# Optimization experiments

Measured on AMD Instinct MI355X. Metric: run time of the kernel, lower is better.

Reference implementation:

```python
import jax, jax.numpy as jnp
import numpy as np

N = 100000      # nodes
E = 3200000     # edges
F_IN = 78       # num_features_mol
F_GAT = 256     # mol_out_feats
HEADS = 2
F_HYP = 128     # mol_out_feats_hyper


def setup_inputs() -> dict:
    key = jax.random.key(0)
    ks = jax.random.split(key, 32)
    g = lambda k, s: jax.random.normal(k, s, dtype=jnp.float32) * 0.05
    inp = {}
    inp["mol_x"] = jax.random.normal(ks[0], (N, F_IN), dtype=jnp.float32)
    inp["mol_edge_index"] = jax.random.randint(ks[1], (2, E), 0, N)
    inp["hyper_edge"] = jax.random.randint(ks[2], (2, E), 0, N)
    # GAT layer 1 (78 -> 256, 2 heads, concat=False)
    inp["W1"] = g(ks[3], (F_IN, HEADS * F_GAT)); inp["as1"] = g(ks[4], (HEADS, F_GAT)); inp["ad1"] = g(ks[5], (HEADS, F_GAT)); inp["b1"] = jnp.zeros((F_GAT,), jnp.float32)
    # GAT layers 2,3 (256 -> 256)
    inp["W2"] = g(ks[6], (F_GAT, HEADS * F_GAT)); inp["as2"] = g(ks[7], (HEADS, F_GAT)); inp["ad2"] = g(ks[8], (HEADS, F_GAT)); inp["b2"] = jnp.zeros((F_GAT,), jnp.float32)
    inp["W3"] = g(ks[9], (F_GAT, HEADS * F_GAT)); inp["as3"] = g(ks[10], (HEADS, F_GAT)); inp["ad3"] = g(ks[11], (HEADS, F_GAT)); inp["b3"] = jnp.zeros((F_GAT,), jnp.float32)
    # GRU-style gating fusion
    inp["fc1_w"] = g(ks[12], (F_GAT, F_GAT)); inp["fc1_b"] = jnp.zeros((F_GAT,), jnp.float32)
    inp["fc2_w"] = g(ks[13], (F_GAT, F_GAT)); inp["fc2_b"] = jnp.zeros((F_GAT,), jnp.float32)
    inp["mol_bias"] = jax.random.uniform(ks[14], (1, F_GAT), jnp.float32, -0.2, 0.2)
    # HypergraphConv layers (334 -> 128 -> 128)
    inp["theta1"] = g(ks[15], (F_GAT + F_IN, F_HYP)); inp["hb1"] = jnp.zeros((F_HYP,), jnp.float32)
    inp["theta2"] = g(ks[16], (F_HYP, F_HYP)); inp["hb2"] = jnp.zeros((F_HYP,), jnp.float32)
    return inp


def _gat(x, src, dst, W, a_s, a_d, b):
    # PyG GATConv, heads=2, concat=False, eval mode (no dropout), self-loops pre-added in src/dst
    xh = (x @ W).reshape(N, HEADS, F_GAT)            # [N,H,C]
    a_src = (xh * a_s).sum(-1)                        # [N,H]
    a_dst = (xh * a_d).sum(-1)                        # [N,H]
    e = jax.nn.leaky_relu(a_src[src] + a_dst[dst], 0.2)  # [E',H]
    m = jax.ops.segment_max(e, dst, num_segments=N)
    ex = jnp.exp(e - m[dst])
    s = jax.ops.segment_sum(ex, dst, num_segments=N)
    alpha = ex / s[dst]                               # softmax over incoming edges
    out = jax.ops.segment_sum(xh[src] * alpha[:, :, None], dst, num_segments=N)
    return out.mean(axis=1) + b                       # concat=False -> head mean


def _hyper(x, node, edge, theta, b):
    # PyG HypergraphConv, use_attention=False: D^-1 H B^-1 H^T X Theta + b
    xt = x @ theta
    ones = jnp.ones((node.shape[0],), xt.dtype)
    D = jax.ops.segment_sum(ones, node, num_segments=N)
    B = jax.ops.segment_sum(ones, edge, num_segments=N)
    Dinv = jnp.where(D > 0, 1.0 / D, 0.0)
    Binv = jnp.where(B > 0, 1.0 / B, 0.0)
    ef = Binv[:, None] * jax.ops.segment_sum(xt[node], edge, num_segments=N)
    nf = Dinv[:, None] * jax.ops.segment_sum(ef[edge], node, num_segments=N)
    return nf + b


def _forward(mol_x, mol_edge_index, hyper_edge,
             W1, as1, ad1, b1, W2, as2, ad2, b2, W3, as3, ad3, b3,
             fc1_w, fc1_b, fc2_w, fc2_b, mol_bias, theta1, hb1, theta2, hb2):
    loops = jnp.arange(N, dtype=mol_edge_index.dtype)
    src = jnp.concatenate([mol_edge_index[0], loops])
    dst = jnp.concatenate([mol_edge_index[1], loops])
    hyper_x0 = jax.lax.stop_gradient(mol_x)  # .clone().detach()
    # layer 0
    h = jax.nn.relu(_gat(mol_x, src, dst, W1, as1, ad1, b1))
    # layer 1 (relu) + gate
    x = jax.nn.relu(_gat(h, src, dst, W2, as2, ad2, b2))
    z = jax.nn.sigmoid(x @ fc1_w.T + fc1_b + h @ fc2_w.T + fc2_b + mol_bias)
    h = z * x + (1.0 - z) * h
    # layer 2 (no relu) + gate
    x = _gat(h, src, dst, W3, as3, ad3, b3)
    z = jax.nn.sigmoid(x @ fc1_w.T + fc1_b + h @ fc2_w.T + fc2_b + mol_bias)
    h = z * x + (1.0 - z) * h
    # hypergraph branch (source uses mol_edge_index here, hyper_edge is unused)
    hx = jnp.concatenate([jax.lax.stop_gradient(h), hyper_x0], axis=1)
    node, edge = mol_edge_index[0], mol_edge_index[1]
    hx = jax.nn.relu(_hyper(hx, node, edge, theta1, hb1))
    hx = jax.nn.relu(_hyper(hx, node, edge, theta2, hb2))
    return jnp.concatenate([h, hx], axis=1)  # [N, 384]


def reference(mol_x, mol_edge_index, hyper_edge,
              W1, as1, ad1, b1, W2, as2, ad2, b2, W3, as3, ad3, b3,
              fc1_w, fc1_b, fc2_w, fc2_b, mol_bias, theta1, hb1, theta2, hb2):
    return _forward(mol_x, mol_edge_index, hyper_edge,
                    W1, as1, ad1, b1, W2, as2, ad2, b2, W3, as3, ad3, b3,
                    fc1_w, fc1_b, fc2_w, fc2_b, mol_bias, theta1, hb1, theta2, hb2)
```

## Files before the change

### kernel.cpp

```cpp
#include <hip/hip_runtime.h>

typedef unsigned short u16;
typedef __attribute__((ext_vector_type(8))) short short8v;
typedef __attribute__((ext_vector_type(8))) unsigned short ushort8v;
typedef __attribute__((ext_vector_type(4))) unsigned short ushort4v;
typedef __attribute__((ext_vector_type(4))) float f32x4;

__device__ __forceinline__ float bf2f(u16 u) {
    union { unsigned int i; float f; } v; v.i = ((unsigned int)u) << 16; return v.f;
}
__device__ __forceinline__ u16 f2bf(float f) {
    union { float f; unsigned int i; } v; v.f = f;
    unsigned int i = v.i;
    return (u16)((i + 0x7FFFu + ((i >> 16) & 1u)) >> 16);
}
__device__ __forceinline__ float leaky02(float x) { return x > 0.f ? x : 0.2f * x; }
__device__ __forceinline__ float load_in(const void* p, long i, int isbf) {
    return isbf ? bf2f(((const u16*)p)[i]) : ((const float*)p)[i];
}

__global__ void detect_kernel(const unsigned* __restrict__ w, int* __restrict__ flag) {
    __shared__ int cnt;
    int t = threadIdx.x;
    if (t == 0) cnt = 0;
    __syncthreads();
    unsigned x = w[t * 16];
    unsigned lo = x & 0xFFFFu;
    int e = (int)((x >> 7) & 0xFFu);
    int good = (lo == 0u) || (e >= 100 && e <= 140);
    atomicAdd(&cnt, good);
    __syncthreads();
    if (t == 0) *flag = (cnt > 128) ? 1 : 0;
}

#define CSR_NBK 1024

__global__ __launch_bounds__(256)
void bucket_count_kernel(const int* __restrict__ ei, int* __restrict__ bcs,
                         int* __restrict__ bcd, int E_, int n, int SH) {
    __shared__ int hs[CSR_NBK], hd[CSR_NBK];
    const int t = threadIdx.x;
    for (int i = t; i < CSR_NBK; i += 256) { hs[i] = 0; hd[i] = 0; }
    __syncthreads();
    const int e0 = blockIdx.x * 4096;
    #pragma unroll
    for (int k = 0; k < 16; ++k) {
        int e = e0 + k * 256 + t;
        if (e < E_) {
            int s = ei[e], d = ei[E_ + e];
            if ((unsigned)s >= (unsigned)n) s = 0;
            if ((unsigned)d >= (unsigned)n) d = 0;
            atomicAdd(&hs[s >> SH], 1);
            atomicAdd(&hd[d >> SH], 1);
        }
    }
    __syncthreads();
    for (int i = t; i < CSR_NBK; i += 256) {
        if (hs[i]) atomicAdd(&bcs[i], hs[i]);
        if (hd[i]) atomicAdd(&bcd[i], hd[i]);
    }
}

__global__ void scan_excl_kernel(const int* __restrict__ deg, int* __restrict__ ptr, int n) {
    __shared__ int s_woff[17];
    __shared__ int s_carry;
    const int t = threadIdx.x;
    const int lane = t & 63, wid = t >> 6;
    if (t == 0) s_carry = 0;
    __syncthreads();
    for (int base = 0; base < n; base += 1024) {
        int i = base + t;
        int v = (i < n) ? deg[i] : 0;
        int incl = v;
        #pragma unroll
        for (int d = 1; d < 64; d <<= 1) {
            int x = __shfl_up(incl, d, 64);
            if (lane >= d) incl += x;
        }
        if (lane == 63) s_woff[wid] = incl;
        __syncthreads();
        if (t == 0) {
            int run = 0;
            #pragma unroll
            for (int w = 0; w < 16; ++w) { int x = s_woff[w]; s_woff[w] = run; run += x; }
            s_woff[16] = run;
        }
        __syncthreads();
        int excl = s_carry + s_woff[wid] + incl - v;
        if (i < n) ptr[i] = excl;
        __syncthreads();
        if (t == 0) s_carry += s_woff[16];
        __syncthreads();
    }
    if (t == 0) ptr[n] = s_carry;
}

__global__ void copy2_kernel(const int* __restrict__ a, int* __restrict__ b,
                             const int* __restrict__ c, int* __restrict__ d2, int n) {
    int i = blockIdx.x * 256 + threadIdx.x;
    if (i < n) { b[i] = a[i]; d2[i] = c[i]; }
}

__global__ __launch_bounds__(256)
void partition_kernel(const int* __restrict__ ei, int* __restrict__ bcur_s,
                      int* __restrict__ bcur_d, int2* __restrict__ ps,
                      int2* __restrict__ pd, int E_, int n, int SH) {
    __shared__ int cs[CSR_NBK], cd[CSR_NBK], bs[CSR_NBK], bd[CSR_NBK];
    const int t = threadIdx.x;
    for (int i = t; i < CSR_NBK; i += 256) { cs[i] = 0; cd[i] = 0; }
    __syncthreads();
    const int e0 = blockIdx.x * 4096;
    int sv[16], dv[16];
    #pragma unroll
    for (int k = 0; k < 16; ++k) {
        int e = e0 + k * 256 + t;
        int s = -1, d = 0;
        if (e < E_) {
            s = ei[e]; d = ei[E_ + e];
            if ((unsigned)s >= (unsigned)n) s = 0;
            if ((unsigned)d >= (unsigned)n) d = 0;
            atomicAdd(&cs[s >> SH], 1);
            atomicAdd(&cd[d >> SH], 1);
        }
        sv[k] = (e < E_) ? s : -1;
        dv[k] = d;
    }
    __syncthreads();
    for (int i = t; i < CSR_NBK; i += 256) {
        bs[i] = cs[i] ? atomicAdd(&bcur_s[i], cs[i]) : 0;
        bd[i] = cd[i] ? atomicAdd(&bcur_d[i], cd[i]) : 0;
        cs[i] = 0; cd[i] = 0;
    }
    __syncthreads();
    #pragma unroll
    for (int k = 0; k < 16; ++k) {
        int s = sv[k];
        if (s < 0) continue;
        int d = dv[k];
        int p = bs[s >> SH] + atomicAdd(&cs[s >> SH], 1);
        ps[p] = make_int2(d, s);
        int q = bd[d >> SH] + atomicAdd(&cd[d >> SH], 1);
        pd[q] = make_int2(s, d);
    }
}

__global__ __launch_bounds__(256)
void fill_bucket_kernel(const int2* __restrict__ pairs, const int* __restrict__ bptr,
                        int* __restrict__ ptr, int* __restrict__ idx, int n, int SH) {
    __shared__ int cnt[256];
    __shared__ int wsum[5];
    const int b = blockIdx.x;
    const int n0 = b << SH;
    if (n0 >= n) return;
    const int nn = min(1 << SH, n - n0);
    const int t = threadIdx.x;
    cnt[t] = 0;
    __syncthreads();
    const int pbeg = bptr[b], pend = bptr[b + 1];
    for (int j = pbeg + t; j < pend; j += 256)
        atomicAdd(&cnt[pairs[j].y - n0], 1);
    __syncthreads();
    const int c = (t < nn) ? cnt[t] : 0;
    int v = c;
    const int lane = t & 63, wid = t >> 6;
    #pragma unroll
    for (int d = 1; d < 64; d <<= 1) {
        int x = __shfl_up(v, d, 64);
        if (lane >= d) v += x;
    }
    if (lane == 63) wsum[wid] = v;
    __syncthreads();
    if (t == 0) {
        int r = 0;
        #pragma unroll
        for (int w = 0; w < 4; ++w) { int x = wsum[w]; wsum[w] = r; r += x; }
        wsum[4] = r;
    }
    __syncthreads();
    v += wsum[wid];
    const int excl = pbeg + v - c;
    __syncthreads();
    if (t < nn) { cnt[t] = excl; ptr[n0 + t] = excl; }
    if (t == 0 && n0 + nn == n) ptr[n] = pbeg + wsum[4];
    __syncthreads();
    for (int j = pbeg + t; j < pend; j += 256) {
        int2 pr = pairs[j];
        int p = atomicAdd(&cnt[pr.y - n0], 1);
        idx[p] = pr.x;
    }
}

__global__ void ingest_transpose_kernel(const void* __restrict__ src, long base,
                                        u16* __restrict__ dst, int K, int Nc, int Kp,
                                        const int* __restrict__ flag) {
    int i = blockIdx.x * 256 + threadIdx.x;
    if (i >= Nc * Kp) return;
    int n = i / Kp, k = i - n * Kp;
    float v = (k < K) ? load_in(src, base + (long)k * Nc + n, *flag) : 0.f;
    dst[i] = f2bf(v);
}

__global__ void ingest_copy_kernel(const void* __restrict__ src, u16* __restrict__ dst,
                                   int n, const int* __restrict__ flag) {
    int i = blockIdx.x * 256 + threadIdx.x;
    if (i < n) dst[i] = f2bf(load_in(src, i, *flag));
}

__global__ void ingest_wcat_kernel(const void* __restrict__ W, u16* __restrict__ dst,
                                   int Kin, int Fh, const int* __restrict__ flag) {
    int i = blockIdx.x * 256 + threadIdx.x;
    int tot = 256 * 2 * Fh;
    if (i >= tot) return;
    int o = i / (2 * Fh), k = i - o * 2 * Fh;
    int h = k / Fh, c = k - h * Fh;
    float v = (c < Kin) ? 0.5f * load_in(W, (long)c * 512 + h * 256 + o, *flag) : 0.f;
    dst[i] = f2bf(v);
}

__global__ void ingest_bcat_kernel(const void* __restrict__ fc1, const void* __restrict__ fc2,
                                   u16* __restrict__ dst, const int* __restrict__ flag) {
    int i = blockIdx.x * 256 + threadIdx.x;
    if (i >= 256 * 512) return;
    int o = i >> 9, k = i & 511;
    float v = (k < 256) ? load_in(fc1, (long)o * 256 + k, *flag)
                        : load_in(fc2, (long)o * 256 + k - 256, *flag);
    dst[i] = f2bf(v);
}

__global__ void ingest_pad_molx_kernel(const void* __restrict__ x, u16* __restrict__ dst,
                                       int ldd, int total, const int* __restrict__ flag) {
    int i = blockIdx.x * 256 + threadIdx.x;
    if (i >= total) return;
    int r = i / 96, c = i - r * 96;
    float v = (c < 78) ? load_in(x, (long)r * 78 + c, *flag) : 0.f;
    dst[(size_t)r * ldd + c] = f2bf(v);
}

__global__ void attn_vec_kernel(const void* __restrict__ W, const void* __restrict__ as_,
                                const void* __restrict__ ad_, float* __restrict__ was,
                                float* __restrict__ wad, int Kin, int Fh,
                                const int* __restrict__ flag) {
    int i = blockIdx.x * 256 + threadIdx.x;
    if (i >= 2 * Fh) return;
    int h = i / Fh, c = i - h * Fh;
    float s = 0.f, d = 0.f;
    if (c < Kin) {
        int f = *flag;
        for (int o = 0; o < 256; ++o) {
            float w = load_in(W, (long)c * 512 + h * 256 + o, f);
            s += w * load_in(as_, h * 256 + o, f);
            d += w * load_in(ad_, h * 256 + o, f);
        }
    }
    was[i] = s; wad[i] = d;
}

__global__ __launch_bounds__(256, 2)
void gemm_kernel(const u16* __restrict__ A, int lda,
                 const u16* __restrict__ Bt, int ldb,
                 u16* __restrict__ C, int ldc, int K, int M, int beta,
                 const u16* __restrict__ bias, int relu) {
    __shared__ __align__(16) u16 As[128 * 32];
    __shared__ __align__(16) u16 Bs[128 * 32];
    const int tid = threadIdx.x;
    const int wave = tid >> 6, lane = tid & 63;
    const int m0 = blockIdx.x * 128;
    const int n0 = blockIdx.y * 128;
    const int wm = (wave & 1) * 64, wn = (wave >> 1) * 64;
    const int r = lane & 15, q = lane >> 4;

    f32x4 acc[4][4];
    if (beta) {
        #pragma unroll
        for (int i = 0; i < 4; ++i)
            #pragma unroll
            for (int j = 0; j < 4; ++j)
                #pragma unroll
                for (int rr = 0; rr < 4; ++rr) {
                    size_t gr = (size_t)(m0 + wm + 16 * i + q * 4 + rr);
                    int gc = n0 + wn + 16 * j + r;
                    acc[i][j][rr] = bf2f(C[gr * ldc + gc]);
                }
    } else {
        #pragma unroll
        for (int i = 0; i < 4; ++i)
            #pragma unroll
            for (int j = 0; j < 4; ++j) acc[i][j] = (f32x4)0.f;
    }

    const int rowT = wave * 16 + (lane >> 2);
    const int koff = (lane & 3) * 8;
    int rA0 = m0 + rowT;       if (rA0 > M - 1) rA0 = M - 1;
    int rA1 = m0 + rowT + 64;  if (rA1 > M - 1) rA1 = M - 1;
    const u16* gA0 = A + (size_t)rA0 * lda + koff;
    const u16* gA1 = A + (size_t)rA1 * lda + koff;
    const u16* gB0 = Bt + (size_t)(n0 + rowT) * ldb + koff;
    const u16* gB1 = Bt + (size_t)(n0 + rowT + 64) * ldb + koff;
    u16* sA0 = &As[rowT * 32 + koff];
    u16* sA1 = &As[(rowT + 64) * 32 + koff];
    u16* sB0 = &Bs[rowT * 32 + koff];
    u16* sB1 = &Bs[(rowT + 64) * 32 + koff];

    const int nK = K >> 5;
    for (int kt = 0; kt < nK; ++kt) {
        ushort8v ta0 = *(const ushort8v*)gA0;
        ushort8v ta1 = *(const ushort8v*)gA1;
        ushort8v tb0 = *(const ushort8v*)gB0;
        ushort8v tb1 = *(const ushort8v*)gB1;
        gA0 += 32; gA1 += 32; gB0 += 32; gB1 += 32;
        __syncthreads();
        *(ushort8v*)sA0 = ta0;
        *(ushort8v*)sA1 = ta1;
        *(ushort8v*)sB0 = tb0;
        *(ushort8v*)sB1 = tb1;
        __syncthreads();
        short8v af[4], bf[4];
        #pragma unroll
        for (int i = 0; i < 4; ++i) af[i] = *(const short8v*)&As[(wm + 16 * i + r) * 32 + q * 8];
        #pragma unroll
        for (int j = 0; j < 4; ++j) bf[j] = *(const short8v*)&Bs[(wn + 16 * j + r) * 32 + q * 8];
        #pragma unroll
        for (int i = 0; i < 4; ++i)
            #pragma unroll
            for (int j = 0; j < 4; ++j)
                acc[i][j] = __builtin_amdgcn_mfma_f32_16x16x32_bf16(af[i], bf[j], acc[i][j], 0, 0, 0);
    }
    #pragma unroll
    for (int j = 0; j < 4; ++j) {
        int gc = n0 + wn + 16 * j + r;
        float bv = bias ? bf2f(bias[gc]) : 0.f;
        #pragma unroll
        for (int i = 0; i < 4; ++i)
            #pragma unroll
            for (int rr = 0; rr < 4; ++rr) {
                size_t gr = (size_t)(m0 + wm + 16 * i + q * 4 + rr);
                float x = acc[i][j][rr] + bv;
                if (relu) x = fmaxf(x, 0.f);
                C[gr * ldc + gc] = f2bf(x);
            }
    }
}

__global__ __launch_bounds__(256)
void attn_dots_h_kernel(const u16* __restrict__ hsrc, int ldh,
                        const float* __restrict__ was, const float* __restrict__ wad,
                        float* __restrict__ a_src, float* __restrict__ a_dst,
                        int Fh, int n) {
    int v = blockIdx.x * 4 + (threadIdx.x >> 6);
    if (v >= n) return;
    const int lane = threadIdx.x & 63;
    const int c0 = lane * 4;
    float ps0 = 0.f, pd0 = 0.f, ps1 = 0.f, pd1 = 0.f;
    if (c0 < Fh) {
        ushort4v xv = *(const ushort4v*)&hsrc[(size_t)v * ldh + c0];
        #pragma unroll
        for (int k = 0; k < 4; ++k) {
            float x = bf2f(xv[k]);
            ps0 += x * was[c0 + k];
            pd0 += x * wad[c0 + k];
            ps1 += x * was[Fh + c0 + k];
            pd1 += x * wad[Fh + c0 + k];
        }
    }
    #pragma unroll
    for (int d = 1; d < 64; d <<= 1) {
        ps0 += __shfl_xor(ps0, d, 64); pd0 += __shfl_xor(pd0, d, 64);
        ps1 += __shfl_xor(ps1, d, 64); pd1 += __shfl_xor(pd1, d, 64);
    }
    if (lane == 0) {
        a_src[2 * v] = ps0; a_src[2 * v + 1] = ps1;
        a_dst[2 * v] = pd0; a_dst[2 * v + 1] = pd1;
    }
}

__global__ __launch_bounds__(256)
void gat_agg_h_kernel(const u16* __restrict__ hsrc, int ldh, int F,
                      const float* __restrict__ asrc, const float* __restrict__ adst,
                      const int* __restrict__ ptr, const int* __restrict__ idx,
                      u16* __restrict__ agg, int ldagg, int n, int Etot) {
    int v = blockIdx.x * 4 + (threadIdx.x >> 6);
    if (v >= n) return;
    const int lane = threadIdx.x & 63;
    const int sub = lane >> 5;
    const int c0 = (lane & 31) * 8;
    const int act = (c0 < F);
    int beg = ptr[v], end = ptr[v + 1];
    beg = min(max(beg, 0), Etot);
    end = min(max(end, beg), Etot);
    const float ad0 = adst[2 * v], ad1 = adst[2 * v + 1];
    const float es0 = leaky02(asrc[2 * v] + ad0);
    const float es1 = leaky02(asrc[2 * v + 1] + ad1);
    float m0 = es0, m1 = es1;
    for (int j = beg + lane; j < end; j += 64) {
        int s = idx[j]; s = ((unsigned)s < (unsigned)n) ? s : 0;
        m0 = fmaxf(m0, leaky02(asrc[2 * s] + ad0));
        m1 = fmaxf(m1, leaky02(asrc[2 * s + 1] + ad1));
    }
    #pragma unroll
    for (int d = 1; d < 64; d <<= 1) {
        m0 = fmaxf(m0, __shfl_xor(m0, d, 64));
        m1 = fmaxf(m1, __shfl_xor(m1, d, 64));
    }
    float s0 = 0.f, s1 = 0.f;
    for (int j = beg + lane; j < end; j += 64) {
        int s = idx[j]; s = ((unsigned)s < (unsigned)n) ? s : 0;
        s0 += __expf(leaky02(asrc[2 * s] + ad0) - m0);
        s1 += __expf(leaky02(asrc[2 * s + 1] + ad1) - m1);
    }
    #pragma unroll
    for (int d = 1; d < 64; d <<= 1) { s0 += __shfl_xor(s0, d, 64); s1 += __shfl_xor(s1, d, 64); }
    s0 += __expf(es0 - m0);
    s1 += __expf(es1 - m1);
    float f0a[8] = {0,0,0,0,0,0,0,0};
    float f1a[8] = {0,0,0,0,0,0,0,0};
    int j = beg + sub;
    for (; j + 2 < end; j += 4) {
        int sA = idx[j];     sA = ((unsigned)sA < (unsigned)n) ? sA : 0;
        int sB = idx[j + 2]; sB = ((unsigned)sB < (unsigned)n) ? sB : 0;
        float wA0 = __expf(leaky02(asrc[2 * sA] + ad0) - m0);
        float wA1 = __expf(leaky02(asrc[2 * sA + 1] + ad1) - m1);
        float wB0 = __expf(leaky02(asrc[2 * sB] + ad0) - m0);
        float wB1 = __expf(leaky02(asrc[2 * sB + 1] + ad1) - m1);
        if (act) {
            ushort8v fA = *(const ushort8v*)&hsrc[(size_t)sA * ldh + c0];
            ushort8v fB = *(const ushort8v*)&hsrc[(size_t)sB * ldh + c0];
            #pragma unroll
            for (int k = 0; k < 8; ++k) {
                float xA = bf2f(fA[k]), xB = bf2f(fB[k]);
                f0a[k] += wA0 * xA + wB0 * xB;
                f1a[k] += wA1 * xA + wB1 * xB;
            }
        }
    }
    for (; j < end; j += 2) {
        int s = idx[j]; s = ((unsigned)s < (unsigned)n) ? s : 0;
        float w0 = __expf(leaky02(asrc[2 * s] + ad0) - m0);
        float w1 = __expf(leaky02(asrc[2 * s + 1] + ad1) - m1);
        if (act) {
            ushort8v f = *(const ushort8v*)&hsrc[(size_t)s * ldh + c0];
            #pragma unroll
            for (int k = 0; k < 8; ++k) {
                float x = bf2f(f[k]);
                f0a[k] += w0 * x;
                f1a[k] += w1 * x;
            }
        }
    }
    if (sub == 0 && act) {
        float w0 = __expf(es0 - m0), w1 = __expf(es1 - m1);
        ushort8v f = *(const ushort8v*)&hsrc[(size_t)v * ldh + c0];
        #pragma unroll
        for (int k = 0; k < 8; ++k) {
            float x = bf2f(f[k]);
            f0a[k] += w0 * x;
            f1a[k] += w1 * x;
        }
    }
    #pragma unroll
    for (int k = 0; k < 8; ++k) {
        f0a[k] += __shfl_xor(f0a[k], 32, 64);
        f1a[k] += __shfl_xor(f1a[k], 32, 64);
    }
    if (lane < 32 && act) {
        const float i0 = 1.f / s0, i1 = 1.f / s1;
        ushort8v o0, o1;
        #pragma unroll
        for (int k = 0; k < 8; ++k) { o0[k] = f2bf(f0a[k] * i0); o1[k] = f2bf(f1a[k] * i1); }
        *(ushort8v*)&agg[(size_t)v * ldagg + c0] = o0;
        *(ushort8v*)&agg[(size_t)v * ldagg + F + c0] = o1;
    }
}

__global__ __launch_bounds__(256)
void gate_kernel(const u16* __restrict__ logit, const u16* __restrict__ cat,
                 const u16* __restrict__ fc1b, const u16* __restrict__ fc2b,
                 const u16* __restrict__ molb, u16* __restrict__ dest,
                 void* __restrict__ outw, const int* __restrict__ flag, int n) {
    int i = blockIdx.x * 256 + threadIdx.x;
    if (i >= n) return;
    int node = i >> 5, c0 = (i & 31) * 8;
    ushort8v lg = *(const ushort8v*)&logit[(size_t)node * 256 + c0];
    ushort8v xv = *(const ushort8v*)&cat[(size_t)node * 512 + c0];
    ushort8v hv = *(const ushort8v*)&cat[(size_t)node * 512 + 256 + c0];
    ushort8v b1v = *(const ushort8v*)&fc1b[c0];
    ushort8v b2v = *(const ushort8v*)&fc2b[c0];
    ushort8v mbv = *(const ushort8v*)&molb[c0];
    float ov[8];
    ushort8v dv;
    #pragma unroll
    for (int k = 0; k < 8; ++k) {
        float l = bf2f(lg[k]) + bf2f(b1v[k]) + bf2f(b2v[k]) + bf2f(mbv[k]);
        float z = 1.f / (1.f + __expf(-l));
        ov[k] = z * bf2f(xv[k]) + (1.f - z) * bf2f(hv[k]);
        dv[k] = f2bf(ov[k]);
    }
    *(ushort8v*)&dest[(size_t)node * 512 + c0] = dv;
    if (outw) {
        if (*flag) {
            *(ushort8v*)((u16*)outw + (size_t)node * 384 + c0) = dv;
        } else {
            float* o = (float*)outw + (size_t)node * 384 + c0;
            #pragma unroll
            for (int k = 0; k < 8; ++k) o[k] = ov[k];
        }
    }
}

__global__ __launch_bounds__(256)
void hyper_gather_kernel(const u16* __restrict__ feat, const int* __restrict__ ptr,
                         const int* __restrict__ idx, const u16* __restrict__ bias,
                         u16* __restrict__ outb, int ldo, void* __restrict__ outw,
                         int col0, const int* __restrict__ flag,
                         int do_relu, int n, int Etot) {
    int v = blockIdx.x * 4 + (threadIdx.x >> 6);
    if (v >= n) return;
    const int lane = threadIdx.x & 63;
    const int c0 = (lane & 15) * 8, sub = lane >> 4;
    int beg = ptr[v], end = ptr[v + 1];
    beg = min(max(beg, 0), Etot);
    end = min(max(end, beg), Etot);
    const float inv = (end > beg) ? 1.f / (float)(end - beg) : 0.f;
    float acc[8] = {0,0,0,0,0,0,0,0};
    for (int j = beg + sub; j < end; j += 4) {
        int s = idx[j]; s = ((unsigned)s < (unsigned)n) ? s : 0;
        ushort8v f = *(const ushort8v*)&feat[(size_t)s * 128 + c0];
        #pragma unroll
        for (int k = 0; k < 8; ++k) acc[k] += bf2f(f[k]);
    }
    #pragma unroll
    for (int k = 0; k < 8; ++k) {
        acc[k] += __shfl_xor(acc[k], 16, 64);
        acc[k] += __shfl_xor(acc[k], 32, 64);
    }
    if (sub == 0) {
        float ov[8];
        ushort8v o;
        #pragma unroll
        for (int k = 0; k < 8; ++k) {
            float x = acc[k] * inv + (bias ? bf2f(bias[c0 + k]) : 0.f);
            if (do_relu) x = fmaxf(x, 0.f);
            ov[k] = x;
            o[k] = f2bf(x);
        }
        if (outb) *(ushort8v*)&outb[(size_t)v * ldo + c0] = o;
        if (outw) {
            if (*flag) {
                *(ushort8v*)((u16*)outw + (size_t)v * 384 + col0 + c0) = o;
            } else {
                float* ofp = (float*)outw + (size_t)v * 384 + col0 + c0;
                #pragma unroll
                for (int k = 0; k < 8; ++k) ofp[k] = ov[k];
            }
        }
    }
}

extern "C" void kernel_launch(void* const* d_in, const int* in_sizes, int n_in,
                              void* d_out, int out_size, void* d_ws, size_t ws_size,
                              hipStream_t stream) {
    const void* molx = d_in[0];
    const int*  ei   = (const int*)d_in[1];
    const void* W1 = d_in[3], *as1 = d_in[4], *ad1 = d_in[5], *b1 = d_in[6];
    const void* W2 = d_in[7], *as2 = d_in[8], *ad2 = d_in[9], *b2 = d_in[10];
    const void* W3 = d_in[11], *as3 = d_in[12], *ad3 = d_in[13], *b3 = d_in[14];
    const void* fc1w = d_in[15], *fc1b = d_in[16], *fc2w = d_in[17], *fc2b = d_in[18];
    const void* molb = d_in[19];
    const void* th1 = d_in[20], *hb1 = d_in[21], *th2 = d_in[22], *hb2 = d_in[23];
    (void)n_in; (void)out_size;

    const int N = in_sizes[0] / 78;
    const int E = in_sizes[1] / 2;
    const int Mp = ((N + 127) / 128) * 128;

    int SH = 0;
    while (((N - 1) >> SH) >= CSR_NBK) SH++;

    char* base = (char*)d_ws;
    size_t off = 0;
    auto alloc = [&](size_t bytes) -> void* {
        void* r = base + off;
        off = (off + bytes + 255) & ~(size_t)255;
        return r;
    };
    int* flag = (int*)alloc(4);
    u16* bv1 = (u16*)alloc(256 * 2); u16* bv2 = (u16*)alloc(256 * 2); u16* bv3 = (u16*)alloc(256 * 2);
    u16* fc1bv = (u16*)alloc(256 * 2); u16* fc2bv = (u16*)alloc(256 * 2); u16* molbv = (u16*)alloc(256 * 2);
    u16* hb1v = (u16*)alloc(128 * 2); u16* hb2v = (u16*)alloc(128 * 2);
    float* was1 = (float*)alloc(192 * 4); float* wad1 = (float*)alloc(192 * 4);
    float* was2 = (float*)alloc(512 * 4); float* wad2 = (float*)alloc(512 * 4);
    float* was3 = (float*)alloc(512 * 4); float* wad3 = (float*)alloc(512 * 4);
    u16* Wc1 = (u16*)alloc(256 * 192 * 2);
    u16* Wc2 = (u16*)alloc(256 * 512 * 2);
    u16* Wc3 = (u16*)alloc(256 * 512 * 2);
    u16* Bcat = (u16*)alloc(256 * 512 * 2);
    u16* th1ta = (u16*)alloc(128 * 256 * 2);
    u16* th1tb = (u16*)alloc(128 * 96 * 2);
    u16* th2t  = (u16*)alloc(128 * 128 * 2);
    float* a_src = (float*)alloc((size_t)N * 2 * 4);
    float* a_dst = (float*)alloc((size_t)N * 2 * 4);
    int* ptr_src = (int*)alloc((size_t)(N + 1) * 4);
    int* ptr_dst = (int*)alloc((size_t)(N + 1) * 4);
    int* bcnt_src = (int*)alloc(CSR_NBK * 4);
    int* bcnt_dst = (int*)alloc(CSR_NBK * 4);
    int* bptr_src = (int*)alloc((CSR_NBK + 1) * 4);
    int* bptr_dst = (int*)alloc((CSR_NBK + 1) * 4);
    int* bcur_src = (int*)alloc(CSR_NBK * 4);
    int* bcur_dst = (int*)alloc(CSR_NBK * 4);
    int* idx_src = (int*)alloc((size_t)E * 4);
    int* idx_dst = (int*)alloc((size_t)E * 4);
    u16* cat = (u16*)alloc((size_t)Mp * 512 * 2);
    u16* agg = (u16*)alloc((size_t)Mp * 512 * 2);
    u16* xt   = agg;
    u16* efb  = agg + (size_t)Mp * 128;
    u16* hx1  = agg + (size_t)Mp * 256;
    u16* mxp2 = agg + (size_t)Mp * 384;

    int2* pairs_src; int2* pairs_dst;
    if (off + (size_t)E * 16 + 1024 <= ws_size) {
        pairs_src = (int2*)alloc((size_t)E * 8);
        pairs_dst = (int2*)alloc((size_t)E * 8);
    } else {
        pairs_src = (int2*)agg;
        pairs_dst = (int2*)((char*)agg + (size_t)E * 8);
    }

    const int nodeBlocks = (N + 3) / 4;
    const int eTiles = (E + 4095) / 4096;

    detect_kernel<<<1, 256, 0, stream>>>((const unsigned*)molx, flag);

    hipMemsetAsync(bcnt_src, 0, CSR_NBK * 4, stream);
    hipMemsetAsync(bcnt_dst, 0, CSR_NBK * 4, stream);
    bucket_count_kernel<<<eTiles, 256, 0, stream>>>(ei, bcnt_src, bcnt_dst, E, N, SH);
    scan_excl_kernel<<<1, 1024, 0, stream>>>(bcnt_src, bptr_src, CSR_NBK);
    scan_excl_kernel<<<1, 1024, 0, stream>>>(bcnt_dst, bptr_dst, CSR_NBK);
    copy2_kernel<<<(CSR_NBK + 255) / 256, 256, 0, stream>>>(bptr_src, bcur_src, bptr_dst, bcur_dst, CSR_NBK);
    partition_kernel<<<eTiles, 256, 0, stream>>>(ei, bcur_src, bcur_dst,
                                                 pairs_src, pairs_dst, E, N, SH);
    fill_bucket_kernel<<<CSR_NBK, 256, 0, stream>>>(pairs_src, bptr_src, ptr_src, idx_src, N, SH);
    fill_bucket_kernel<<<CSR_NBK, 256, 0, stream>>>(pairs_dst, bptr_dst, ptr_dst, idx_dst, N, SH);

    ingest_wcat_kernel<<<(256 * 192 + 255) / 256, 256, 0, stream>>>(W1, Wc1, 78, 96, flag);
    ingest_wcat_kernel<<<(256 * 512 + 255) / 256, 256, 0, stream>>>(W2, Wc2, 256, 256, flag);
    ingest_wcat_kernel<<<(256 * 512 + 255) / 256, 256, 0, stream>>>(W3, Wc3, 256, 256, flag);
    ingest_bcat_kernel<<<(256 * 512 + 255) / 256, 256, 0, stream>>>(fc1w, fc2w, Bcat, flag);
    ingest_transpose_kernel<<<(128 * 256 + 255) / 256, 256, 0, stream>>>(th1, 0, th1ta, 256, 128, 256, flag);
    ingest_transpose_kernel<<<(128 * 96 + 255) / 256, 256, 0, stream>>>(th1, (long)256 * 128, th1tb, 78, 128, 96, flag);
    ingest_transpose_kernel<<<(128 * 128 + 255) / 256, 256, 0, stream>>>(th2, 0, th2t, 128, 128, 128, flag);
    attn_vec_kernel<<<1, 256, 0, stream>>>(W1, as1, ad1, was1, wad1, 78, 96, flag);
    attn_vec_kernel<<<2, 256, 0, stream>>>(W2, as2, ad2, was2, wad2, 256, 256, flag);
    attn_vec_kernel<<<2, 256, 0, stream>>>(W3, as3, ad3, was3, wad3, 256, 256, flag);
    ingest_copy_kernel<<<1, 256, 0, stream>>>(b1, bv1, 256, flag);
    ingest_copy_kernel<<<1, 256, 0, stream>>>(b2, bv2, 256, flag);
    ingest_copy_kernel<<<1, 256, 0, stream>>>(b3, bv3, 256, flag);
    ingest_copy_kernel<<<1, 256, 0, stream>>>(fc1b, fc1bv, 256, flag);
    ingest_copy_kernel<<<1, 256, 0, stream>>>(fc2b, fc2bv, 256, flag);
    ingest_copy_kernel<<<1, 256, 0, stream>>>(molb, molbv, 256, flag);
    ingest_copy_kernel<<<1, 128, 0, stream>>>(hb1, hb1v, 128, flag);
    ingest_copy_kernel<<<1, 128, 0, stream>>>(hb2, hb2v, 128, flag);
    ingest_pad_molx_kernel<<<(N * 96 + 255) / 256, 256, 0, stream>>>(molx, cat, 512, N * 96, flag);

    auto gemm = [&](const u16* A, int lda, const u16* Bt, int ldb, u16* C, int ldc,
                    int K, int Nc, int M, int beta, const u16* bias, int relu) {
        dim3 g(Mp / 128, Nc / 128);
        gemm_kernel<<<g, 256, 0, stream>>>(A, lda, Bt, ldb, C, ldc, K, M, beta, bias, relu);
    };

    attn_dots_h_kernel<<<nodeBlocks, 256, 0, stream>>>(cat, 512, was1, wad1, a_src, a_dst, 96, N);
    gat_agg_h_kernel<<<nodeBlocks, 256, 0, stream>>>(cat, 512, 96, a_src, a_dst,
                                                     ptr_dst, idx_dst, agg, 192, N, E);
    gemm(agg, 192, Wc1, 192, cat + 256, 512, 192, 256, Mp, 0, bv1, 1);
    attn_dots_h_kernel<<<nodeBlocks, 256, 0, stream>>>(cat + 256, 512, was2, wad2, a_src, a_dst, 256, N);
    gat_agg_h_kernel<<<nodeBlocks, 256, 0, stream>>>(cat + 256, 512, 256, a_src, a_dst,
                                                     ptr_dst, idx_dst, agg, 512, N, E);
    gemm(agg, 512, Wc2, 512, cat, 512, 512, 256, Mp, 0, bv2, 1);
    gemm(cat, 512, Bcat, 512, agg , 256, 512, 256, Mp, 0, nullptr, 0);
    gate_kernel<<<(N * 32 + 255) / 256, 256, 0, stream>>>(agg, cat, fc1bv, fc2bv, molbv,
                                                          cat + 256, nullptr, flag, N * 32);
    attn_dots_h_kernel<<<nodeBlocks, 256, 0, stream>>>(cat + 256, 512, was3, wad3, a_src, a_dst, 256, N);
    gat_agg_h_kernel<<<nodeBlocks, 256, 0, stream>>>(cat + 256, 512, 256, a_src, a_dst,
                                                     ptr_dst, idx_dst, agg, 512, N, E);
    gemm(agg, 512, Wc3, 512, cat, 512, 512, 256, Mp, 0, bv3, 0);
    gemm(cat, 512, Bcat, 512, agg , 256, 512, 256, Mp, 0, nullptr, 0);
    gate_kernel<<<(N * 32 + 255) / 256, 256, 0, stream>>>(agg, cat, fc1bv, fc2bv, molbv,
                                                          cat + 256, d_out, flag, N * 32);
    ingest_pad_molx_kernel<<<(N * 96 + 255) / 256, 256, 0, stream>>>(molx, mxp2, 96, N * 96, flag);
    gemm(cat + 256, 512, th1ta, 256, xt, 128, 256, 128, Mp, 0, nullptr, 0);
    gemm(mxp2, 96, th1tb, 96, xt, 128, 96, 128, Mp, 1, nullptr, 0);
    hyper_gather_kernel<<<nodeBlocks, 256, 0, stream>>>(xt, ptr_dst, idx_dst, (const u16*)nullptr,
                                                        efb, 128, nullptr, 0, flag, 0, N, E);
    hyper_gather_kernel<<<nodeBlocks, 256, 0, stream>>>(efb, ptr_src, idx_src, hb1v,
                                                        hx1, 128, nullptr, 0, flag, 1, N, E);
    gemm(hx1, 128, th2t, 128, xt, 128, 128, 128, Mp, 0, nullptr, 0);
    hyper_gather_kernel<<<nodeBlocks, 256, 0, stream>>>(xt, ptr_dst, idx_dst, (const u16*)nullptr,
                                                        efb, 128, nullptr, 0, flag, 0, N, E);
    hyper_gather_kernel<<<nodeBlocks, 256, 0, stream>>>(efb, ptr_src, idx_src, hb2v,
                                                        (u16*)nullptr, 0, d_out, 256, flag, 1, N, E);
}
```

Baseline: 2.320 ms.

## Single-pass online softmax GAT aggregation with packed FMA and bpermute weight sharing

Rewrites the GAT neighbour aggregation as a single pass over edges in 64-edge chunks. Each lane computes one edge's score, and the kernel keeps a running max with rescaling (online softmax), replacing the three separate passes over idx/asrc. Edge indices and weights are broadcast to feature sub-groups via ds_bpermute. Accumulation uses v_pk_fma_f32 on packed bf16 pairs, with a templated group count (4 groups for the 96-wide layer). The hypergraph gather is also unrolled by two and switched to v_pk_add_f32. This adds rescaling work per chunk and relies on inline asm.

Measured after the change: 2.150 ms. -7.3%, faster.

```diff
diff --git a/kernel.cpp b/kernel.cpp
--- a/kernel.cpp
+++ b/kernel.cpp
@@ -5,6 +5,7 @@
 typedef __attribute__((ext_vector_type(8))) unsigned short ushort8v;
 typedef __attribute__((ext_vector_type(4))) unsigned short ushort4v;
 typedef __attribute__((ext_vector_type(4))) float f32x4;
+typedef __attribute__((ext_vector_type(2))) float f32x2;
 
 __device__ __forceinline__ float bf2f(u16 u) {
     union { unsigned int i; float f; } v; v.i = ((unsigned int)u) << 16; return v.f;
@@ -17,6 +18,28 @@
 __device__ __forceinline__ float leaky02(float x) { return x > 0.f ? x : 0.2f * x; }
 __device__ __forceinline__ float load_in(const void* p, long i, int isbf) {
     return isbf ? bf2f(((const u16*)p)[i]) : ((const float*)p)[i];
+}
+__device__ __forceinline__ f32x2 pk_fma(f32x2 a, f32x2 b, f32x2 c) {
+    f32x2 d;
+    asm("v_pk_fma_f32 %0, %1, %2, %3" : "=v"(d) : "v"(a), "v"(b), "v"(c));
+    return d;
+}
+__device__ __forceinline__ f32x2 pk_add(f32x2 a, f32x2 b) {
+    f32x2 d;
+    asm("v_pk_add_f32 %0, %1, %2" : "=v"(d) : "v"(a), "v"(b));
+    return d;
+}
+__device__ __forceinline__ f32x2 bfpair(unsigned int d) {
+    union { unsigned int i; float f; } lo, hi;
+    lo.i = d << 16;
+    hi.i = d & 0xFFFF0000u;
+    f32x2 r; r.x = lo.f; r.y = hi.f; return r;
+}
+__device__ __forceinline__ float bperm_f(int addr, float v) {
+    return __int_as_float(__builtin_amdgcn_ds_bpermute(addr, __float_as_int(v)));
+}
+__device__ __forceinline__ int bperm_i(int addr, int v) {
+    return __builtin_amdgcn_ds_bpermute(addr, v);
 }
 
 __global__ void detect_kernel(const unsigned* __restrict__ w, int* __restrict__ flag) {
@@ -373,16 +396,18 @@
     }
 }
 
+template <int NG>
 __global__ __launch_bounds__(256)
 void gat_agg_h_kernel(const u16* __restrict__ hsrc, int ldh, int F,
                       const float* __restrict__ asrc, const float* __restrict__ adst,
                       const int* __restrict__ ptr, const int* __restrict__ idx,
                       u16* __restrict__ agg, int ldagg, int n, int Etot) {
+    constexpr int GL = 64 / NG;
     int v = blockIdx.x * 4 + (threadIdx.x >> 6);
     if (v >= n) return;
     const int lane = threadIdx.x & 63;
-    const int sub = lane >> 5;
-    const int c0 = (lane & 31) * 8;
+    const int sub = lane / GL;
+    const int c0 = (lane & (GL - 1)) * 8;
     const int act = (c0 < F);
     int beg = ptr[v], end = ptr[v + 1];
     beg = min(max(beg, 0), Etot);
@@ -391,81 +416,102 @@
     const float es0 = leaky02(asrc[2 * v] + ad0);
     const float es1 = leaky02(asrc[2 * v + 1] + ad1);
     float m0 = es0, m1 = es1;
-    for (int j = beg + lane; j < end; j += 64) {
-        int s = idx[j]; s = ((unsigned)s < (unsigned)n) ? s : 0;
-        m0 = fmaxf(m0, leaky02(asrc[2 * s] + ad0));
-        m1 = fmaxf(m1, leaky02(asrc[2 * s + 1] + ad1));
+    float s0 = 0.f, s1 = 0.f;
+    f32x2 f0p[4], f1p[4];
+    #pragma unroll
+    for (int p = 0; p < 4; ++p) { f0p[p] = (f32x2)0.f; f1p[p] = (f32x2)0.f; }
+
+    for (int cb = beg; cb < end; cb += 64) {
+        const int cnt = min(64, end - cb);
+        int sE = 0;
+        float sc0 = -1e30f, sc1 = -1e30f;
+        if (lane < cnt) {
+            sE = idx[cb + lane];
+            sE = ((unsigned)sE < (unsigned)n) ? sE : 0;
+            sc0 = leaky02(asrc[2 * sE] + ad0);
+            sc1 = leaky02(asrc[2 * sE + 1] + ad1);
+        }
+        float cm0 = sc0, cm1 = sc1;
+        #pragma unroll
+        for (int d = 1; d < 64; d <<= 1) {
+            cm0 = fmaxf(cm0, __shfl_xor(cm0, d, 64));
+            cm1 = fmaxf(cm1, __shfl_xor(cm1, d, 64));
+        }
+        const float nm0 = fmaxf(m0, cm0), nm1 = fmaxf(m1, cm1);
+        const float r0 = __expf(m0 - nm0), r1 = __expf(m1 - nm1);
+        m0 = nm0; m1 = nm1;
+        s0 *= r0; s1 *= r1;
+        #pragma unroll
+        for (int p = 0; p < 4; ++p) {
+            f0p[p].x *= r0; f0p[p].y *= r0;
+            f1p[p].x *= r1; f1p[p].y *= r1;
+        }
+        float wE0 = 0.f, wE1 = 0.f;
+        if (lane < cnt) {
+            wE0 = __expf(sc0 - m0);
+            wE1 = __expf(sc1 - m1);
+            s0 += wE0; s1 += wE1;
+        }
+        const int nIt = (cnt + 2 * NG - 1) / (2 * NG);
+        int jj = sub;
+        for (int it = 0; it < nIt; ++it, jj += 2 * NG) {
+            const int aA = jj * 4, aB = aA + NG * 4;
+            const int sA = bperm_i(aA, sE);
+            const float wA0 = bperm_f(aA, wE0), wA1 = bperm_f(aA, wE1);
+            const int sB = bperm_i(aB, sE);
+            const float wB0 = bperm_f(aB, wE0), wB1 = bperm_f(aB, wE1);
+            if (act) {
+                const uint4 fA = *(const uint4*)&hsrc[(size_t)sA * ldh + c0];
+                const uint4 fB = *(const uint4*)&hsrc[(size_t)sB * ldh + c0];
+                const f32x2 wA0v = {wA0, wA0}, wA1v = {wA1, wA1};
+                const f32x2 wB0v = {wB0, wB0}, wB1v = {wB1, wB1};
+                #pragma unroll
+                for (int p = 0; p < 4; ++p) {
+                    const f32x2 xA = bfpair(((const unsigned*)&fA)[p]);
+                    const f32x2 xB = bfpair(((const unsigned*)&fB)[p]);
+                    f0p[p] = pk_fma(xA, wA0v, f0p[p]);
+                    f1p[p] = pk_fma(xA, wA1v, f1p[p]);
+                    f0p[p] = pk_fma(xB, wB0v, f0p[p]);
+                    f1p[p] = pk_fma(xB, wB1v, f1p[p]);
+                }
+            }
+        }
     }
     #pragma unroll
     for (int d = 1; d < 64; d <<= 1) {
-        m0 = fmaxf(m0, __shfl_xor(m0, d, 64));
-        m1 = fmaxf(m1, __shfl_xor(m1, d, 64));
-    }
-    float s0 = 0.f, s1 = 0.f;
-    for (int j = beg + lane; j < end; j += 64) {
-        int s = idx[j]; s = ((unsigned)s < (unsigned)n) ? s : 0;
-        s0 += __expf(leaky02(asrc[2 * s] + ad0) - m0);
-        s1 += __expf(leaky02(asrc[2 * s + 1] + ad1) - m1);
-    }
-    #pragma unroll
-    for (int d = 1; d < 64; d <<= 1) { s0 += __shfl_xor(s0, d, 64); s1 += __shfl_xor(s1, d, 64); }
-    s0 += __expf(es0 - m0);
-    s1 += __expf(es1 - m1);
-    float f0a[8] = {0,0,0,0,0,0,0,0};
-    float f1a[8] = {0,0,0,0,0,0,0,0};
-    int j = beg + sub;
-    for (; j + 2 < end; j += 4) {
-        int sA = idx[j];     sA = ((unsigned)sA < (unsigned)n) ? sA : 0;
-        int sB = idx[j + 2]; sB = ((unsigned)sB < (unsigned)n) ? sB : 0;
-        float wA0 = __expf(leaky02(asrc[2 * sA] + ad0) - m0);
-        float wA1 = __expf(leaky02(asrc[2 * sA + 1] + ad1) - m1);
-        float wB0 = __expf(leaky02(asrc[2 * sB] + ad0) - m0);
-        float wB1 = __expf(leaky02(asrc[2 * sB + 1] + ad1) - m1);
-        if (act) {
-            ushort8v fA = *(const ushort8v*)&hsrc[(size_t)sA * ldh + c0];
-            ushort8v fB = *(const ushort8v*)&hsrc[(size_t)sB * ldh + c0];
-            #pragma unroll
-            for (int k = 0; k < 8; ++k) {
-                float xA = bf2f(fA[k]), xB = bf2f(fB[k]);
-                f0a[k] += wA0 * xA + wB0 * xB;
-                f1a[k] += wA1 * xA + wB1 * xB;
-            }
-        }
-    }
-    for (; j < end; j += 2) {
-        int s = idx[j]; s = ((unsigned)s < (unsigned)n) ? s : 0;
-        float w0 = __expf(leaky02(asrc[2 * s] + ad0) - m0);
-        float w1 = __expf(leaky02(asrc[2 * s + 1] + ad1) - m1);
-        if (act) {
-            ushort8v f = *(const ushort8v*)&hsrc[(size_t)s * ldh + c0];
-            #pragma unroll
-            for (int k = 0; k < 8; ++k) {
-                float x = bf2f(f[k]);
-                f0a[k] += w0 * x;
-                f1a[k] += w1 * x;
-            }
-        }
-    }
+        s0 += __shfl_xor(s0, d, 64);
+        s1 += __shfl_xor(s1, d, 64);
+    }
+    const float w0s = __expf(es0 - m0), w1s = __expf(es1 - m1);
+    s0 += w0s; s1 += w1s;
     if (sub == 0 && act) {
-        float w0 = __expf(es0 - m0), w1 = __expf(es1 - m1);
-        ushort8v f = *(const ushort8v*)&hsrc[(size_t)v * ldh + c0];
-        #pragma unroll
-        for (int k = 0; k < 8; ++k) {
-            float x = bf2f(f[k]);
-            f0a[k] += w0 * x;
-            f1a[k] += w1 * x;
-        }
-    }
-    #pragma unroll
-    for (int k = 0; k < 8; ++k) {
-        f0a[k] += __shfl_xor(f0a[k], 32, 64);
-        f1a[k] += __shfl_xor(f1a[k], 32, 64);
-    }
-    if (lane < 32 && act) {
+        const uint4 f = *(const uint4*)&hsrc[(size_t)v * ldh + c0];
+        const f32x2 w0v = {w0s, w0s}, w1v = {w1s, w1s};
+        #pragma unroll
+        for (int p = 0; p < 4; ++p) {
+            const f32x2 x = bfpair(((const unsigned*)&f)[p]);
+            f0p[p] = pk_fma(x, w0v, f0p[p]);
+            f1p[p] = pk_fma(x, w1v, f1p[p]);
+        }
+    }
+    #pragma unroll
+    for (int p = 0; p < 4; ++p) {
+        #pragma unroll
+        for (int d = GL; d < 64; d <<= 1) {
+            f0p[p].x += __shfl_xor(f0p[p].x, d, 64);
+            f0p[p].y += __shfl_xor(f0p[p].y, d, 64);
+            f1p[p].x += __shfl_xor(f1p[p].x, d, 64);
+            f1p[p].y += __shfl_xor(f1p[p].y, d, 64);
+        }
+    }
+    if (lane < GL && act) {
         const float i0 = 1.f / s0, i1 = 1.f / s1;
         ushort8v o0, o1;
         #pragma unroll
-        for (int k = 0; k < 8; ++k) { o0[k] = f2bf(f0a[k] * i0); o1[k] = f2bf(f1a[k] * i1); }
+        for (int p = 0; p < 4; ++p) {
+            o0[2 * p] = f2bf(f0p[p].x * i0); o0[2 * p + 1] = f2bf(f0p[p].y * i0);
+            o1[2 * p] = f2bf(f1p[p].x * i1); o1[2 * p + 1] = f2bf(f1p[p].y * i1);
+        }
         *(ushort8v*)&agg[(size_t)v * ldagg + c0] = o0;
         *(ushort8v*)&agg[(size_t)v * ldagg + F + c0] = o1;
     }
@@ -520,27 +566,45 @@
     beg = min(max(beg, 0), Etot);
     end = min(max(end, beg), Etot);
     const float inv = (end > beg) ? 1.f / (float)(end - beg) : 0.f;
-    float acc[8] = {0,0,0,0,0,0,0,0};
-    for (int j = beg + sub; j < end; j += 4) {
+    f32x2 a2[4];
+    #pragma unroll
+    for (int p = 0; p < 4; ++p) a2[p] = (f32x2)0.f;
+    int j = beg + sub;
+    for (; j + 4 < end; j += 8) {
+        int sA = idx[j];     sA = ((unsigned)sA < (unsigned)n) ? sA : 0;
+        int sB = idx[j + 4]; sB = ((unsigned)sB < (unsigned)n) ? sB : 0;
+        const uint4 fA = *(const uint4*)&feat[(size_t)sA * 128 + c0];
+        const uint4 fB = *(const uint4*)&feat[(size_t)sB * 128 + c0];
+        #pragma unroll
+        for (int p = 0; p < 4; ++p) {
+            a2[p] = pk_add(a2[p], bfpair(((const unsigned*)&fA)[p]));
+            a2[p] = pk_add(a2[p], bfpair(((const unsigned*)&fB)[p]));
+        }
+    }
+    for (; j < end; j += 4) {
         int s = idx[j]; s = ((unsigned)s < (unsigned)n) ? s : 0;
-        ushort8v f = *(const ushort8v*)&feat[(size_t)s * 128 + c0];
-        #pragma unroll
-        for (int k = 0; k < 8; ++k) acc[k] += bf2f(f[k]);
-    }
-    #pragma unroll
-    for (int k = 0; k < 8; ++k) {
-        acc[k] += __shfl_xor(acc[k], 16, 64);
-        acc[k] += __shfl_xor(acc[k], 32, 64);
+        const uint4 f = *(const uint4*)&feat[(size_t)s * 128 + c0];
+        #pragma unroll
+        for (int p = 0; p < 4; ++p)
+            a2[p] = pk_add(a2[p], bfpair(((const unsigned*)&f)[p]));
+    }
+    #pragma unroll
+    for (int p = 0; p < 4; ++p) {
+        a2[p].x += __shfl_xor(a2[p].x, 16, 64);
+        a2[p].y += __shfl_xor(a2[p].y, 16, 64);
+        a2[p].x += __shfl_xor(a2[p].x, 32, 64);
+        a2[p].y += __shfl_xor(a2[p].y, 32, 64);
     }
     if (sub == 0) {
         float ov[8];
         ushort8v o;
         #pragma unroll
-        for (int k = 0; k < 8; ++k) {
-            float x = acc[k] * inv + (bias ? bf2f(bias[c0 + k]) : 0.f);
-            if (do_relu) x = fmaxf(x, 0.f);
-            ov[k] = x;
-            o[k] = f2bf(x);
+        for (int p = 0; p < 4; ++p) {
+            float x0 = a2[p].x * inv + (bias ? bf2f(bias[c0 + 2 * p]) : 0.f);
+            float x1 = a2[p].y * inv + (bias ? bf2f(bias[c0 + 2 * p + 1]) : 0.f);
+            if (do_relu) { x0 = fmaxf(x0, 0.f); x1 = fmaxf(x1, 0.f); }
+            ov[2 * p] = x0; ov[2 * p + 1] = x1;
+            o[2 * p] = f2bf(x0); o[2 * p + 1] = f2bf(x1);
         }
         if (outb) *(ushort8v*)&outb[(size_t)v * ldo + c0] = o;
         if (outw) {
@@ -667,19 +731,19 @@
     };
 
     attn_dots_h_kernel<<<nodeBlocks, 256, 0, stream>>>(cat, 512, was1, wad1, a_src, a_dst, 96, N);
-    gat_agg_h_kernel<<<nodeBlocks, 256, 0, stream>>>(cat, 512, 96, a_src, a_dst,
-                                                     ptr_dst, idx_dst, agg, 192, N, E);
+    gat_agg_h_kernel<4><<<nodeBlocks, 256, 0, stream>>>(cat, 512, 96, a_src, a_dst,
+                                                        ptr_dst, idx_dst, agg, 192, N, E);
     gemm(agg, 192, Wc1, 192, cat + 256, 512, 192, 256, Mp, 0, bv1, 1);
     attn_dots_h_kernel<<<nodeBlocks, 256, 0, stream>>>(cat + 256, 512, was2, wad2, a_src, a_dst, 256, N);
-    gat_agg_h_kernel<<<nodeBlocks, 256, 0, stream>>>(cat + 256, 512, 256, a_src, a_dst,
-                                                     ptr_dst, idx_dst, agg, 512, N, E);
+    gat_agg_h_kernel<2><<<nodeBlocks, 256, 0, stream>>>(cat + 256, 512, 256, a_src, a_dst,
+                                                        ptr_dst, idx_dst, agg, 512, N, E);
     gemm(agg, 512, Wc2, 512, cat, 512, 512, 256, Mp, 0, bv2, 1);
     gemm(cat, 512, Bcat, 512, agg , 256, 512, 256, Mp, 0, nullptr, 0);
     gate_kernel<<<(N * 32 + 255) / 256, 256, 0, stream>>>(agg, cat, fc1bv, fc2bv, molbv,
                                                           cat + 256, nullptr, flag, N * 32);
     attn_dots_h_kernel<<<nodeBlocks, 256, 0, stream>>>(cat + 256, 512, was3, wad3, a_src, a_dst, 256, N);
-    gat_agg_h_kernel<<<nodeBlocks, 256, 0, stream>>>(cat + 256, 512, 256, a_src, a_dst,
-                                                     ptr_dst, idx_dst, agg, 512, N, E);
+    gat_agg_h_kernel<2><<<nodeBlocks, 256, 0, stream>>>(cat + 256, 512, 256, a_src, a_dst,
+                                                        ptr_dst, idx_dst, agg, 512, N, E);
     gemm(agg, 512, Wc3, 512, cat, 512, 512, 256, Mp, 0, bv3, 0);
     gemm(cat, 512, Bcat, 512, agg , 256, 512, 256, Mp, 0, nullptr, 0);
     gate_kernel<<<(N * 32 + 255) / 256, 256, 0, stream>>>(agg, cat, fc1bv, fc2bv, molbv,
```
